# Performance work log

Hardware: AMD Instinct MI355X
Metric: run time of the kernel (lower is better)

Reference implementation:

```python
import jax, jax.numpy as jnp
import numpy as np

N_NODES = 50000
N_FEAT = 128
DIM = 10
N_EDGES = 1600000
N_GRAPHS = 1000


def setup_inputs() -> dict:
    key = jax.random.key(0)
    ks = jax.random.split(key, 8)
    x = jax.random.normal(ks[0], (N_NODES, N_FEAT), dtype=jnp.float32)
    W1_l = jax.random.normal(ks[1], (DIM, N_FEAT), dtype=jnp.float32) * 0.1
    W1_r = jax.random.normal(ks[2], (DIM, N_FEAT), dtype=jnp.float32) * 0.1
    W2_l = jax.random.normal(ks[3], (DIM, DIM), dtype=jnp.float32) * 0.3
    W2_r = jax.random.normal(ks[4], (DIM, DIM), dtype=jnp.float32) * 0.3
    Wfc = jax.random.normal(ks[5], (1, DIM), dtype=jnp.float32) * 0.3
    edge_index = jax.random.randint(ks[6], (2, N_EDGES), 0, N_NODES, dtype=jnp.int64)
    batch = jnp.sort(jax.random.randint(ks[7], (N_NODES,), 0, N_GRAPHS, dtype=jnp.int64))
    return {"x": x, "W1_l": W1_l, "W1_r": W1_r, "W2_l": W2_l, "W2_r": W2_r,
            "Wfc": Wfc, "edge_index": edge_index, "batch": batch}


def _sage_conv(h, src, dst, deg_inv, Wl, Wr):
    # mean aggregation over incoming neighbors, then two bias-free linears
    agg = jax.ops.segment_sum(h[src], dst, num_segments=N_NODES)  # [N, F]
    agg = agg * deg_inv[:, None]
    return agg @ Wl.T + h @ Wr.T


def reference(x, W1_l, W1_r, W2_l, W2_r, Wfc, edge_index, batch):
    src, dst = edge_index[0], edge_index[1]
    # in-degree per destination node (mean denominator, clamped at 1 like PyG)
    deg = jax.ops.segment_sum(jnp.ones((src.shape[0],), x.dtype), dst, num_segments=N_NODES)
    deg_inv = 1.0 / jnp.maximum(deg, 1.0)

    h = jax.nn.relu(_sage_conv(x, src, dst, deg_inv, W1_l, W1_r))
    h = _sage_conv(h, src, dst, deg_inv, W2_l, W2_r)

    # global mean pool over graphs
    counts = jax.ops.segment_sum(jnp.ones((N_NODES,), x.dtype), batch, num_segments=N_GRAPHS)
    pooled = jax.ops.segment_sum(h, batch, num_segments=N_GRAPHS)
    pooled = pooled / jnp.maximum(counts, 1.0)[:, None]

    return jax.nn.sigmoid(pooled @ Wfc.T)  # [N_GRAPHS, 1]
```

## Files before the change

kernel.cpp:

```cpp
#include <hip/hip_runtime.h>
#include <hip/hip_bf16.h>
#include <math.h>

#define N_NODES  50000
#define N_FEAT   128
#define DIM      10
#define N_EDGES  1600000
#define N_GRAPHS 1000
#define PSTRIDE  16
#define CAP      80
#define BSH      7
#define BNODES   128
#define NBUCK    391
#define BCAP     4608
#define ACHUNK   4096
#define ABLOCKS  ((N_EDGES + ACHUNK - 1) / ACHUNK)
#define PBLOCKS4 ((N_NODES * 4 + 255) / 256)
#define SPLIT    2
#define GSLOTS   128
#define SENT     50000


__device__ __forceinline__ float bf2f(unsigned short u) {
    union { unsigned int i; float f; } v;
    v.i = ((unsigned int)u) << 16;
    return v.f;
}

__device__ __forceinline__ float wload(const void* w, int fm, int i) {
    return fm ? ((const float*)w)[i] : bf2f(((const unsigned short*)w)[i]);
}

__device__ __forceinline__ int iload(const void* p, int im, long long pos) {
    return im ? ((const int*)p)[2 * pos] : ((const int*)p)[pos];
}

__device__ __forceinline__ int probe_fm(const void* W1l) {
    const unsigned short* w = (const unsigned short*)W1l;
    int hits = 0;
#pragma unroll
    for (int i = 0; i < 128; i++) {
        int expo = (w[2 * i] >> 7) & 0xFF;
        hits += (expo >= 0x90) ? 1 : 0;
    }
    return (hits >= 4) ? 1 : 0;
}
__device__ __forceinline__ int probe_im(const void* ei) {
    const unsigned int* e = (const unsigned int*)ei;
    unsigned o = 0;
#pragma unroll
    for (int i = 0; i < 8; i++) o |= e[2 * i + 1];
    return (o == 0) ? 1 : 0;
}

#define ACCUM8(f0)                                                  \
    _Pragma("unroll")                                               \
    for (int d = 0; d < DIM; d++) {                                 \
        _Pragma("unroll")                                           \
        for (int k = 0; k < 8; k++) {                               \
            accl[d] += xf[k] * wl[d * N_FEAT + (f0) + k];           \
            accr[d] += xf[k] * wr[d * N_FEAT + (f0) + k];           \
        }                                                           \
    }

__global__ __launch_bounds__(256) void fusedA_kernel(
    const void* __restrict__ ei, const void* __restrict__ x,
    const void* __restrict__ W1l, const void* __restrict__ W1r,
    int* __restrict__ bcur, unsigned int* __restrict__ bedges,
    float* __restrict__ p, float* __restrict__ q) {
    __shared__ union U {
        struct { int hcnt[NBUCK]; int hbase[NBUCK]; } a;
        struct { float wl[DIM * N_FEAT]; float wr[DIM * N_FEAT]; } b;
    } sh;

    if (blockIdx.x < ABLOCKS) {
        int im = probe_im(ei);
        for (int b = threadIdx.x; b < NBUCK; b += 256) sh.a.hcnt[b] = 0;
        __syncthreads();
        long long e0 = (long long)blockIdx.x * ACHUNK;
        int nE = (int)min((long long)ACHUNK, (long long)N_EDGES - e0);
        for (int i = threadIdx.x; i < nE; i += 256) {
            int d = iload(ei, im, (long long)N_EDGES + e0 + i);
            atomicAdd(&sh.a.hcnt[d >> BSH], 1);
        }
        __syncthreads();
        for (int b = threadIdx.x; b < NBUCK; b += 256) {
            int c = sh.a.hcnt[b];
            sh.a.hbase[b] = c ? atomicAdd(&bcur[b], c) : 0;
            sh.a.hcnt[b] = 0;
        }
        __syncthreads();
        for (int i = threadIdx.x; i < nE; i += 256) {
            int s = iload(ei, im, e0 + i);
            int d = iload(ei, im, (long long)N_EDGES + e0 + i);
            unsigned rec = (unsigned)s | ((unsigned)(d & (BNODES - 1)) << 16) | ((unsigned)(d >> BSH) << 23);
            int b = d >> BSH;
            int pos = sh.a.hbase[b] + atomicAdd(&sh.a.hcnt[b], 1);
            if (pos < BCAP) bedges[(size_t)b * BCAP + pos] = rec;
        }
    } else {
        int fm = probe_fm(W1l);
        if (blockIdx.x == ABLOCKS && threadIdx.x < PSTRIDE)
            p[(size_t)SENT * PSTRIDE + threadIdx.x] = 0.f;
        float* wl = sh.b.wl;
        float* wr = sh.b.wr;
        for (int i = threadIdx.x; i < DIM * N_FEAT; i += 256) {
            wl[i] = wload(W1l, fm, i);
            wr[i] = wload(W1r, fm, i);
        }
        __syncthreads();
        int tid4 = (blockIdx.x - ABLOCKS) * 256 + threadIdx.x;
        int n = tid4 >> 2;
        int sub = tid4 & 3;
        if (n >= N_NODES) return;

        float accl[DIM], accr[DIM];
#pragma unroll
        for (int d = 0; d < DIM; d++) { accl[d] = 0.f; accr[d] = 0.f; }

        if (fm) {
            const float4* xr = reinterpret_cast<const float4*>((const float*)x + (size_t)n * N_FEAT);
#pragma unroll
            for (int j = 0; j < 4; j++) {
                int fb = j * 4 + sub;
                float4 v0 = xr[2 * fb];
                float4 v1 = xr[2 * fb + 1];
                float xf[8] = {v0.x, v0.y, v0.z, v0.w, v1.x, v1.y, v1.z, v1.w};
                ACCUM8(fb * 8)
            }
        } else {
            const uint4* xr = reinterpret_cast<const uint4*>((const unsigned short*)x + (size_t)n * N_FEAT);
#pragma unroll
            for (int j = 0; j < 4; j++) {
                int fb = j * 4 + sub;
                uint4 v = xr[fb];
                float xf[8];
                xf[0] = bf2f((unsigned short)(v.x & 0xffff)); xf[1] = bf2f((unsigned short)(v.x >> 16));
                xf[2] = bf2f((unsigned short)(v.y & 0xffff)); xf[3] = bf2f((unsigned short)(v.y >> 16));
                xf[4] = bf2f((unsigned short)(v.z & 0xffff)); xf[5] = bf2f((unsigned short)(v.z >> 16));
                xf[6] = bf2f((unsigned short)(v.w & 0xffff)); xf[7] = bf2f((unsigned short)(v.w >> 16));
                ACCUM8(fb * 8)
            }
        }
#pragma unroll
        for (int d = 0; d < DIM; d++) {
            accl[d] += __shfl_xor(accl[d], 1, 4);
            accl[d] += __shfl_xor(accl[d], 2, 4);
            accr[d] += __shfl_xor(accr[d], 1, 4);
            accr[d] += __shfl_xor(accr[d], 2, 4);
        }
        if (sub == 0) {
            float4* pr = reinterpret_cast<float4*>(p + (size_t)n * PSTRIDE);
            float4* qr = reinterpret_cast<float4*>(q + (size_t)n * PSTRIDE);
            pr[0] = make_float4(accl[0], accl[1], accl[2], accl[3]);
            pr[1] = make_float4(accl[4], accl[5], accl[6], accl[7]);
            pr[2] = make_float4(accl[8], accl[9], 0.f, 0.f);
            pr[3] = make_float4(0.f, 0.f, 0.f, 0.f);
            qr[0] = make_float4(accr[0], accr[1], accr[2], accr[3]);
            qr[1] = make_float4(accr[4], accr[5], accr[6], accr[7]);
            qr[2] = make_float4(accr[8], accr[9], 0.f, 0.f);
            qr[3] = make_float4(0.f, 0.f, 0.f, 0.f);
        }
    }
}

__global__ __launch_bounds__(512) void pullB_kernel(
    const int* __restrict__ bcur, const unsigned int* __restrict__ bedges,
    const float* __restrict__ p, const float* __restrict__ q,
    const void* __restrict__ W1l, const void* __restrict__ W2l,
    const void* __restrict__ W2r, const void* __restrict__ Wfc,
    float* __restrict__ t, float* __restrict__ u, float* __restrict__ dinv) {
    __shared__ unsigned short lcol[BNODES * CAP];
    __shared__ int lcnt[BNODES];
    __shared__ float svl[16], svr[16];
    int fm = probe_fm(W1l);
    if (threadIdx.x < 16) {
        float al = 0.f, ar = 0.f;
        if (threadIdx.x < DIM) {
            for (int i = 0; i < DIM; i++) {
                float w = wload(Wfc, fm, i);
                al += w * wload(W2l, fm, i * DIM + threadIdx.x);
                ar += w * wload(W2r, fm, i * DIM + threadIdx.x);
            }
        }
        svl[threadIdx.x] = al;
        svr[threadIdx.x] = ar;
    }
    const unsigned int s2 = (unsigned)SENT | ((unsigned)SENT << 16);
    uint4 sv = make_uint4(s2, s2, s2, s2);
    uint4* l4 = reinterpret_cast<uint4*>(lcol);
    for (int i = threadIdx.x; i < BNODES * CAP * 2 / 16; i += 512) l4[i] = sv;
    if (threadIdx.x < BNODES) lcnt[threadIdx.x] = 0;
    __syncthreads();

    int b = blockIdx.x;
    int m = min(bcur[b], BCAP);
    const unsigned int* seg = bedges + (size_t)b * BCAP;
    for (int i = threadIdx.x; i < m; i += 512) {
        unsigned rec = seg[i];
        int nidx = (rec >> 16) & (BNODES - 1);
        int pos = atomicAdd(&lcnt[nidx], 1);
        if (pos < CAP) lcol[nidx * CAP + pos] = (unsigned short)(rec & 0xffffu);
    }
    __syncthreads();

    int n = threadIdx.x >> 2;
    int sub4 = (threadIdx.x & 3) * 4;
    int g = (b << BSH) + n;
    if (g >= N_NODES) return;
    int deg = lcnt[n];
    int dcl = min(deg, CAP);
    const unsigned short* cl = lcol + n * CAP;
    float ax = 0.f, ay = 0.f, az = 0.f, aw = 0.f;
    for (int k0 = 0; k0 < dcl; k0 += 8) {
        uint4 cv = *reinterpret_cast<const uint4*>(cl + k0);
        unsigned c[8];
        c[0] = cv.x & 0xffff; c[1] = cv.x >> 16;
        c[2] = cv.y & 0xffff; c[3] = cv.y >> 16;
        c[4] = cv.z & 0xffff; c[5] = cv.z >> 16;
        c[6] = cv.w & 0xffff; c[7] = cv.w >> 16;
#pragma unroll
        for (int j = 0; j < 8; j++) {
            const float4 v = *reinterpret_cast<const float4*>(p + (size_t)c[j] * PSTRIDE + sub4);
            ax += v.x; ay += v.y; az += v.z; aw += v.w;
        }
    }
    float di = 1.0f / fmaxf((float)deg, 1.0f);
    float4 qv  = *reinterpret_cast<const float4*>(q + (size_t)g * PSTRIDE + sub4);
    float4 vlv = *reinterpret_cast<const float4*>(svl + sub4);
    float4 vrv = *reinterpret_cast<const float4*>(svr + sub4);
    float hx = fmaxf(ax * di + qv.x, 0.f);
    float hy = fmaxf(ay * di + qv.y, 0.f);
    float hz = fmaxf(az * di + qv.z, 0.f);
    float hw = fmaxf(aw * di + qv.w, 0.f);
    float tv = hx * vlv.x + hy * vlv.y + hz * vlv.z + hw * vlv.w;
    float uv = hx * vrv.x + hy * vrv.y + hz * vrv.z + hw * vrv.w;
    tv += __shfl_xor(tv, 1, 4); tv += __shfl_xor(tv, 2, 4);
    uv += __shfl_xor(uv, 1, 4); uv += __shfl_xor(uv, 2, 4);
    if ((threadIdx.x & 3) == 0) {
        t[g] = tv;
        u[g] = uv;
        dinv[g] = di;
    }
}

__global__ __launch_bounds__(256) void pull2B_kernel(
    const int* __restrict__ bcur, const unsigned int* __restrict__ bedges,
    const float* __restrict__ t, const float* __restrict__ u,
    const float* __restrict__ dinv, const void* __restrict__ batch,
    const void* __restrict__ ei,
    float* __restrict__ gsum, float* __restrict__ gcnt) {
    __shared__ float lnode[BNODES];
    __shared__ float ldinv[BNODES];
    __shared__ int   lb[BNODES];
    __shared__ float lgs[GSLOTS];
    __shared__ float lgc[GSLOTS];
    int im = probe_im(ei);
    int b = blockIdx.x / SPLIT;
    int s = blockIdx.x % SPLIT;
    int tid = threadIdx.x;
    int node0 = b << BSH;
    int nvalid = min(BNODES, N_NODES - node0);
    if (tid < BNODES) lnode[tid] = 0.f;
    if (tid < nvalid) {
        ldinv[tid] = dinv[node0 + tid];
        lb[tid] = iload(batch, im, node0 + tid);
    }
    if (tid < GSLOTS) { lgs[tid] = 0.f; lgc[tid] = 0.f; }
    __syncthreads();
    int m = min(bcur[b], BCAP);
    int c0 = (m * s) / SPLIT, c1 = (m * (s + 1)) / SPLIT;
    const unsigned int* seg = bedges + (size_t)b * BCAP;
    for (int i = c0 + tid; i < c1; i += 256) {
        unsigned rec = seg[i];
        int src  = rec & 0xffffu;
        int nidx = (rec >> 16) & (BNODES - 1);
        atomicAdd(&lnode[nidx], t[src]);
    }
    __syncthreads();
    int g0 = lb[0];
    int rng = lb[nvalid - 1] - g0 + 1;
    bool useLDS = (rng <= GSLOTS);
    if (tid < nvalid) {
        float gv = lnode[tid] * ldinv[tid];
        if (s == 0) gv += u[node0 + tid];
        int gg = lb[tid];
        if (useLDS) {
            atomicAdd(&lgs[gg - g0], gv);
            if (s == 0) atomicAdd(&lgc[gg - g0], 1.0f);
        } else {
            if (gv != 0.f) atomicAdd(gsum + gg, gv);
            if (s == 0) atomicAdd(gcnt + gg, 1.0f);
        }
    }
    __syncthreads();
    if (useLDS) {
        for (int i = tid; i < rng; i += 256) {
            float v = lgs[i];
            if (v != 0.f) atomicAdd(gsum + g0 + i, v);
            if (s == 0) {
                float c = lgc[i];
                if (c != 0.f) atomicAdd(gcnt + g0 + i, c);
            }
        }
    }
}

__global__ __launch_bounds__(256) void final_kernel(
    const float* __restrict__ gsum, const float* __restrict__ gcnt,
    const void* __restrict__ W1l, void* __restrict__ out) {
    int fm = probe_fm(W1l);
    int g = blockIdx.x * 256 + threadIdx.x;
    if (g >= N_GRAPHS) return;
    float pooled = gsum[g] / fmaxf(gcnt[g], 1.0f);
    float sg = 1.0f / (1.0f + expf(-pooled));
    if (fm) {
        ((float*)out)[g] = sg;
    } else {
        ((__hip_bfloat16*)out)[g] = __float2bfloat16(sg);
    }
}

extern "C" void kernel_launch(void* const* d_in, const int* in_sizes, int n_in,
                              void* d_out, int out_size, void* d_ws, size_t ws_size,
                              hipStream_t stream) {
    const void* x    = d_in[0];
    const void* W1l  = d_in[1];
    const void* W1r  = d_in[2];
    const void* W2l  = d_in[3];
    const void* W2r  = d_in[4];
    const void* Wfc  = d_in[5];
    const void* ei   = d_in[6];
    const void* batc = d_in[7];

    char* ws = (char*)d_ws;
    int*   bcur = (int*)ws;
    float* gsum = (float*)(bcur + NBUCK);
    float* gcnt = gsum + N_GRAPHS;
    unsigned int* bedges = (unsigned int*)(ws + ((((size_t)(gcnt + N_GRAPHS) - (size_t)ws) + 255) & ~(size_t)255));
    float* p    = (float*)(bedges + (size_t)NBUCK * BCAP);
    float* q    = p + (size_t)(N_NODES + 1) * PSTRIDE;
    float* t    = q + (size_t)N_NODES * PSTRIDE;
    float* u    = t + N_NODES;
    float* dinv = u + N_NODES;

    hipMemsetAsync(bcur, 0, (NBUCK + 2 * N_GRAPHS) * sizeof(int), stream);
    fusedA_kernel<<<ABLOCKS + PBLOCKS4, 256, 0, stream>>>(
        ei, x, W1l, W1r, bcur, bedges, p, q);
    pullB_kernel<<<NBUCK, 512, 0, stream>>>(bcur, bedges, p, q,
                                            W1l, W2l, W2r, Wfc, t, u, dinv);
    pull2B_kernel<<<NBUCK * SPLIT, 256, 0, stream>>>(bcur, bedges, t, u, dinv, batc, ei, gsum, gcnt);
    final_kernel<<<(N_GRAPHS + 255) / 256, 256, 0, stream>>>(gsum, gcnt, W1l, d_out);
}
```

Before: 163.9 us.

## Stage edge records in LDS, wave-parallel dtype probes, split pull2 further

The bucketing pass now packs each edge record once into shared memory during the histogram pass and reuses it in the scatter pass, so the edge indices are no longer read from global memory twice. The per-thread serial probes for input dtype (128 loads for float mode, 8 for index width) become one load per lane combined with a wave ballot. The second-layer pull now splits each bucket across four blocks instead of two, for more parallelism at the cost of more global atomics. The 16 KB staging buffer raises shared-memory use in the bucketing blocks, which may reduce occupancy.

Result: faster. 154.6 us (-5.7%).

```diff
diff --git a/kernel.cpp b/kernel.cpp
--- a/kernel.cpp
+++ b/kernel.cpp
@@ -16,7 +16,7 @@
 #define ACHUNK   4096
 #define ABLOCKS  ((N_EDGES + ACHUNK - 1) / ACHUNK)
 #define PBLOCKS4 ((N_NODES * 4 + 255) / 256)
-#define SPLIT    2
+#define SPLIT    4
 #define GSLOTS   128
 #define SENT     50000
 
@@ -35,22 +35,19 @@
     return im ? ((const int*)p)[2 * pos] : ((const int*)p)[pos];
 }
 
-__device__ __forceinline__ int probe_fm(const void* W1l) {
+__device__ __forceinline__ int probe_fm_w(const void* W1l) {
     const unsigned short* w = (const unsigned short*)W1l;
-    int hits = 0;
-#pragma unroll
-    for (int i = 0; i < 128; i++) {
-        int expo = (w[2 * i] >> 7) & 0xFF;
-        hits += (expo >= 0x90) ? 1 : 0;
-    }
-    return (hits >= 4) ? 1 : 0;
-}
-__device__ __forceinline__ int probe_im(const void* ei) {
+    int lane = threadIdx.x & 63;
+    int expo = (w[lane] >> 7) & 0xFF;
+    unsigned long long m = __ballot(expo >= 0x90);
+    return (__popcll(m) >= 4) ? 1 : 0;
+}
+__device__ __forceinline__ int probe_im_w(const void* ei) {
     const unsigned int* e = (const unsigned int*)ei;
-    unsigned o = 0;
-#pragma unroll
-    for (int i = 0; i < 8; i++) o |= e[2 * i + 1];
-    return (o == 0) ? 1 : 0;
+    int lane = threadIdx.x & 63;
+    unsigned v = (lane < 8) ? e[2 * lane + 1] : 0u;
+    unsigned long long m = __ballot(v != 0u);
+    return (m == 0ull) ? 1 : 0;
 }
 
 #define ACCUM8(f0)                                                  \
@@ -69,18 +66,20 @@
     int* __restrict__ bcur, unsigned int* __restrict__ bedges,
     float* __restrict__ p, float* __restrict__ q) {
     __shared__ union U {
-        struct { int hcnt[NBUCK]; int hbase[NBUCK]; } a;
+        struct { unsigned int stage[ACHUNK]; int hcnt[NBUCK]; int hbase[NBUCK]; } a;
         struct { float wl[DIM * N_FEAT]; float wr[DIM * N_FEAT]; } b;
     } sh;
 
     if (blockIdx.x < ABLOCKS) {
-        int im = probe_im(ei);
+        int im = probe_im_w(ei);
         for (int b = threadIdx.x; b < NBUCK; b += 256) sh.a.hcnt[b] = 0;
         __syncthreads();
         long long e0 = (long long)blockIdx.x * ACHUNK;
         int nE = (int)min((long long)ACHUNK, (long long)N_EDGES - e0);
         for (int i = threadIdx.x; i < nE; i += 256) {
+            int s = iload(ei, im, e0 + i);
             int d = iload(ei, im, (long long)N_EDGES + e0 + i);
+            sh.a.stage[i] = (unsigned)s | ((unsigned)(d & (BNODES - 1)) << 16) | ((unsigned)(d >> BSH) << 23);
             atomicAdd(&sh.a.hcnt[d >> BSH], 1);
         }
         __syncthreads();
@@ -91,15 +90,13 @@
         }
         __syncthreads();
         for (int i = threadIdx.x; i < nE; i += 256) {
-            int s = iload(ei, im, e0 + i);
-            int d = iload(ei, im, (long long)N_EDGES + e0 + i);
-            unsigned rec = (unsigned)s | ((unsigned)(d & (BNODES - 1)) << 16) | ((unsigned)(d >> BSH) << 23);
-            int b = d >> BSH;
+            unsigned rec = sh.a.stage[i];
+            int b = rec >> 23;
             int pos = sh.a.hbase[b] + atomicAdd(&sh.a.hcnt[b], 1);
             if (pos < BCAP) bedges[(size_t)b * BCAP + pos] = rec;
         }
     } else {
-        int fm = probe_fm(W1l);
+        int fm = probe_fm_w(W1l);
         if (blockIdx.x == ABLOCKS && threadIdx.x < PSTRIDE)
             p[(size_t)SENT * PSTRIDE + threadIdx.x] = 0.f;
         float* wl = sh.b.wl;
@@ -173,7 +170,7 @@
     __shared__ unsigned short lcol[BNODES * CAP];
     __shared__ int lcnt[BNODES];
     __shared__ float svl[16], svr[16];
-    int fm = probe_fm(W1l);
+    int fm = probe_fm_w(W1l);
     if (threadIdx.x < 16) {
         float al = 0.f, ar = 0.f;
         if (threadIdx.x < DIM) {
@@ -255,7 +252,7 @@
     __shared__ int   lb[BNODES];
     __shared__ float lgs[GSLOTS];
     __shared__ float lgc[GSLOTS];
-    int im = probe_im(ei);
+    int im = probe_im_w(ei);
     int b = blockIdx.x / SPLIT;
     int s = blockIdx.x % SPLIT;
     int tid = threadIdx.x;
@@ -309,7 +306,7 @@
 __global__ __launch_bounds__(256) void final_kernel(
     const float* __restrict__ gsum, const float* __restrict__ gcnt,
     const void* __restrict__ W1l, void* __restrict__ out) {
-    int fm = probe_fm(W1l);
+    int fm = probe_fm_w(W1l);
     int g = blockIdx.x * 256 + threadIdx.x;
     if (g >= N_GRAPHS) return;
     float pooled = gsum[g] / fmaxf(gcnt[g], 1.0f);
```
